# Kernel tuning notes

Hardware: AMD Instinct MI355X
Metric: run time of the kernel (lower is better)

The kernel has to match this reference:

```python
import jax, jax.numpy as jnp
import numpy as np

NEG_INF = -1e9


def setup_inputs() -> dict:
    key = jax.random.key(0)
    ks = jax.random.split(key, 12)
    B, Tq, Tki, E, D, M = 4, 2048, 2048, 1024, 128, 16384
    return {
        "x": jax.random.normal(ks[0], (B, Tq, E), jnp.float32),
        "ki": jax.random.normal(ks[1], (B, Tki, E), jnp.float32),
        "vi": jax.random.normal(ks[2], (B, Tki, E), jnp.float32),
        "mem_keys": jax.random.normal(ks[3], (B, M, D), jnp.float32),
        "mem_vals": jax.random.normal(ks[4], (B, M, D), jnp.float32),
        "Wq": jax.random.normal(ks[5], (E, D), jnp.float32) / np.sqrt(E),
        "bq": jax.random.normal(ks[6], (D,), jnp.float32) * 0.02,
        "Wk": jax.random.normal(ks[7], (E, D), jnp.float32) / np.sqrt(E),
        "bk": jax.random.normal(ks[8], (D,), jnp.float32) * 0.02,
        "Wv": jax.random.normal(ks[9], (E, D), jnp.float32) / np.sqrt(E),
        "bv": jax.random.normal(ks[10], (D,), jnp.float32) * 0.02,
        "gate": jax.random.normal(ks[11], (1,), jnp.float32),
        "idx": 3,
    }


def reference(x, ki, vi, mem_keys, mem_vals, Wq, bq, Wk, bk, Wv, bv, gate, idx):
    B, Tq, E = x.shape
    D = Wq.shape[1]
    top_k = 32
    q = x @ Wq + bq            # [B,Tq,D]
    k = x @ Wk + bk            # [B,Tq,D]
    v = x @ Wv + bv
    s = idx * D                # idx is a python int -> static slice
    k_full = jnp.concatenate([ki[:, :, s:s + D], k], axis=1)   # [B,Tk,D]
    v_full = jnp.concatenate([vi[:, :, s:s + D], v], axis=1)
    Tk = k_full.shape[1]
    # causal SDPA over prefix+current, offset diagonal Tk-Tq
    scores = jnp.einsum("bqd,bkd->bqk", q, k_full) / jnp.sqrt(jnp.float32(D))
    i = jnp.arange(Tq)[:, None]
    j = jnp.arange(Tk)[None, :]
    causal = j <= i + (Tk - Tq)
    scores = jnp.where(causal, scores, NEG_INF)
    att = jax.nn.softmax(scores, axis=-1)
    out = jnp.einsum("bqk,bkd->bqd", att, v_full)              # [B,Tq,D]
    # kNN memory attention: exact top-k inner-product search per query
    mem_scores = jnp.einsum("btd,bmd->btm", q, mem_keys)       # [B,Tq,M]
    _, top_idx = jax.lax.top_k(mem_scores, top_k)              # [B,Tq,K]
    gather = jax.vmap(lambda mem, ix: mem[ix])                 # per batch
    mem_k = gather(mem_keys, top_idx)                          # [B,Tq,K,D]
    mem_v = gather(mem_vals, top_idx)
    # note: original scales by sqrt(Cq)=sqrt(n_embd), not sqrt(head_size)
    mem_att = jax.nn.softmax(
        jnp.einsum("btd,btkd->btk", q, mem_k) / jnp.sqrt(jnp.float32(E)), axis=-1)
    mem_out = jnp.einsum("btk,btkd->btd", mem_att, mem_v)      # [B,Tq,D]
    md_out = out * gate + mem_out * (1.0 - gate)
    return md_out
```

## Files before the change

kernel.cpp:

```cpp
#include <hip/hip_runtime.h>


using bf16x8 = __attribute__((ext_vector_type(8))) short;
using f32x4  = __attribute__((ext_vector_type(4))) float;

typedef __attribute__((address_space(1))) const void GVoid;
typedef __attribute__((address_space(3))) void LVoid;
__device__ __forceinline__ void gl16(const ushort* g, ushort* l) {
  __builtin_amdgcn_global_load_lds((GVoid*)g, (LVoid*)l, 16, 0, 0);
}

__device__ __forceinline__ float bf2f(ushort h) {
  union { uint u; float f; } x; x.u = ((uint)h) << 16; return x.f;
}
__device__ __forceinline__ ushort f2bf(float f) {
  union { float f; uint u; } x; x.f = f;
  uint u = x.u;
  u += 0x7fffu + ((u >> 16) & 1u);
  return (ushort)(u >> 16);
}
__device__ __forceinline__ uint ord2(uint v) {
  uint s = (v >> 15) & 0x00010001u;
  uint t = (s << 15) - s;
  return v ^ t ^ 0x80008000u;
}
__device__ __forceinline__ ushort ord1(ushort h) {
  uint s = (h >> 15) & 1u;
  return (ushort)(h ^ ((s << 15) - s) ^ 0x8000u);
}

__global__ __launch_bounds__(256) void k_wt(const float* __restrict__ Wq,
                                            const float* __restrict__ Wk,
                                            const float* __restrict__ Wv,
                                            ushort* __restrict__ Wth,
                                            ushort* __restrict__ Wtlq) {
  int id = blockIdx.x * 256 + threadIdx.x;
  int z = id >> 17, r = id & 131071;
  int n = r >> 10, k = r & 1023;
  const float* W = (z == 1) ? Wk : (z == 2) ? Wv : Wq;
  float w = W[k * 128 + n];
  ushort h = f2bf(w);
  if (z < 3) Wth[id] = h;
  else       Wtlq[r] = f2bf(w - bf2f(h));
}

__global__ __launch_bounds__(256) void k_cvt8(const float* __restrict__ src,
                                              ushort* __restrict__ dst) {
  int id = blockIdx.x * 256 + threadIdx.x;
  size_t base = (size_t)id * 8;
  float4 a = *(const float4*)(src + base);
  float4 b = *(const float4*)(src + base + 4);
  bf16x8 r;
  r[0] = (short)f2bf(a.x); r[1] = (short)f2bf(a.y);
  r[2] = (short)f2bf(a.z); r[3] = (short)f2bf(a.w);
  r[4] = (short)f2bf(b.x); r[5] = (short)f2bf(b.y);
  r[6] = (short)f2bf(b.z); r[7] = (short)f2bf(b.w);
  *(bf16x8*)(dst + base) = r;
}

__global__ __launch_bounds__(256) void k_xsplit(const float* __restrict__ x,
                                                ushort* __restrict__ xh,
                                                ushort* __restrict__ xl) {
  int id = blockIdx.x * 256 + threadIdx.x;
  size_t base = (size_t)id * 8;
  float4 a = *(const float4*)(x + base);
  float4 b = *(const float4*)(x + base + 4);
  float xf[8] = {a.x, a.y, a.z, a.w, b.x, b.y, b.z, b.w};
  bf16x8 rh, rl;
#pragma unroll
  for (int j = 0; j < 8; ++j) {
    ushort h = f2bf(xf[j]);
    rh[j] = (short)h;
    rl[j] = (short)f2bf(xf[j] - bf2f(h));
  }
  *(bf16x8*)(xh + base) = rh;
  *(bf16x8*)(xl + base) = rl;
}

__global__ __launch_bounds__(256) void k_prefix(const float* __restrict__ ki,
                                                const float* __restrict__ vi,
                                                const int* __restrict__ idx,
                                                ushort* __restrict__ kfull,
                                                ushort* __restrict__ vfull) {
  int s = idx[0] * 128;
  int id = blockIdx.x * 256 + threadIdx.x;
  int d8 = (id & 15) * 8;
  int bt = id >> 4;
  int b = bt >> 11, t = bt & 2047;
  const float* kp = ki + (size_t)bt * 1024 + s + d8;
  const float* vp = vi + (size_t)bt * 1024 + s + d8;
  bf16x8 rk, rv;
#pragma unroll
  for (int j = 0; j < 8; ++j) { rk[j] = (short)f2bf(kp[j]); rv[j] = (short)f2bf(vp[j]); }
  size_t dst = ((size_t)b * 4096 + t) * 128 + d8;
  *(bf16x8*)(kfull + dst) = rk;
  *(bf16x8*)(vfull + dst) = rv;
}

__global__ __launch_bounds__(256) void k_qkv3(const ushort* __restrict__ xh,
                                              const ushort* __restrict__ xl,
                                              const ushort* __restrict__ Wth,
                                              const ushort* __restrict__ Wtlq,
                                              const float* __restrict__ bq,
                                              const float* __restrict__ bk,
                                              const float* __restrict__ bv,
                                              float* __restrict__ qex,
                                              ushort* __restrict__ kfull,
                                              ushort* __restrict__ vfull) {
  __shared__ ushort lds[2][16384];
  int z = blockIdx.z;
  int g = blockIdx.y;
  int m0 = blockIdx.x * 64;
  int tid = threadIdx.x;
  int w = tid >> 6, lane = tid & 63;
  int l15 = lane & 15, q8 = (lane >> 4) * 8;
  const ushort* Wz = Wth + (size_t)z * 131072;
  const ushort* xh_src = xh + (size_t)(m0 + w * 16 + l15) * 1024 + q8;
  const ushort* xl_src = xl + (size_t)(m0 + w * 16 + l15) * 1024 + q8;
  const ushort* wh_src = Wz   + (size_t)(g * 64 + w * 16 + l15) * 1024 + q8;
  const ushort* wl_src = Wtlq + (size_t)(g * 64 + w * 16 + l15) * 1024 + q8;
  int sb = w * 1024;

  f32x4 zero = {0.f, 0.f, 0.f, 0.f};
  f32x4 acc[4] = {zero, zero, zero, zero};

  {
    ushort* B = &lds[0][0];
    gl16(xh_src,      B + sb);
    gl16(xh_src + 32, B + sb + 512);
    gl16(wh_src,      B + 8192 + sb);
    gl16(wh_src + 32, B + 8192 + sb + 512);
    if (z == 0) {
      gl16(xl_src,      B + 4096 + sb);
      gl16(xl_src + 32, B + 4096 + sb + 512);
      gl16(wl_src,      B + 12288 + sb);
      gl16(wl_src + 32, B + 12288 + sb + 512);
    }
  }
  __syncthreads();
  int bf = 0;
  for (int t16 = 0; t16 < 16; ++t16) {
    if (t16 < 15) {
      int k0 = t16 * 64 + 64;
      ushort* B = &lds[bf ^ 1][0];
      gl16(xh_src + k0,      B + sb);
      gl16(xh_src + k0 + 32, B + sb + 512);
      gl16(wh_src + k0,      B + 8192 + sb);
      gl16(wh_src + k0 + 32, B + 8192 + sb + 512);
      if (z == 0) {
        gl16(xl_src + k0,      B + 4096 + sb);
        gl16(xl_src + k0 + 32, B + 4096 + sb + 512);
        gl16(wl_src + k0,      B + 12288 + sb);
        gl16(wl_src + k0 + 32, B + 12288 + sb + 512);
      }
    }
    const ushort* B = &lds[bf][0];
    int lo = lane * 8;
    if (z == 0) {
#pragma unroll
      for (int kc = 0; kc < 2; ++kc) {
        bf16x8 ah = *(const bf16x8*)(B + (w * 2 + kc) * 512 + lo);
        bf16x8 al = *(const bf16x8*)(B + 4096 + (w * 2 + kc) * 512 + lo);
#pragma unroll
        for (int cc = 0; cc < 4; ++cc) {
          bf16x8 bh = *(const bf16x8*)(B + 8192 + (cc * 2 + kc) * 512 + lo);
          bf16x8 bl = *(const bf16x8*)(B + 12288 + (cc * 2 + kc) * 512 + lo);
          acc[cc] = __builtin_amdgcn_mfma_f32_16x16x32_bf16(ah, bh, acc[cc], 0, 0, 0);
          acc[cc] = __builtin_amdgcn_mfma_f32_16x16x32_bf16(ah, bl, acc[cc], 0, 0, 0);
          acc[cc] = __builtin_amdgcn_mfma_f32_16x16x32_bf16(al, bh, acc[cc], 0, 0, 0);
        }
      }
    } else {
#pragma unroll
      for (int kc = 0; kc < 2; ++kc) {
        bf16x8 ah = *(const bf16x8*)(B + (w * 2 + kc) * 512 + lo);
#pragma unroll
        for (int cc = 0; cc < 4; ++cc) {
          bf16x8 bh = *(const bf16x8*)(B + 8192 + (cc * 2 + kc) * 512 + lo);
          acc[cc] = __builtin_amdgcn_mfma_f32_16x16x32_bf16(ah, bh, acc[cc], 0, 0, 0);
        }
      }
    }
    __syncthreads();
    bf ^= 1;
  }

  const float* bias = (z == 0) ? bq : (z == 1) ? bk : bv;
  int mrow = m0 + w * 16 + (lane >> 4) * 4;
#pragma unroll
  for (int cc = 0; cc < 4; ++cc) {
    int n = g * 64 + cc * 16 + l15;
    float bb = bias[n];
#pragma unroll
    for (int r = 0; r < 4; ++r) {
      int m = mrow + r;
      float val = acc[cc][r] + bb;
      if (z == 0) {
        qex[(size_t)m * 128 + n] = val;
      } else {
        int b2 = m >> 11, tt = m & 2047;
        size_t o = ((size_t)b2 * 4096 + 2048 + tt) * 128 + n;
        if (z == 1) kfull[o] = f2bf(val); else vfull[o] = f2bf(val);
      }
    }
  }
}

__global__ __launch_bounds__(256) void k_vt(const ushort* __restrict__ vfull,
                                            ushort* __restrict__ Vt) {
  __shared__ ushort lds[64][136];
  int blk = blockIdx.x;
  int b = blk >> 6, t0 = (blk & 63) * 64;
  int t = threadIdx.x;
#pragma unroll
  for (int p = 0; p < 4; ++p) {
    int ch = p * 256 + t;
    int row = ch >> 4, c8 = (ch & 15) * 8;
    uint4 v = *(const uint4*)(vfull + ((size_t)b * 4096 + t0 + row) * 128 + c8);
    *(uint4*)(&lds[row][c8]) = v;
  }
  __syncthreads();
#pragma unroll
  for (int p = 0; p < 8; ++p) {
    int q = p * 256 + t;
    int d = q >> 4, t4 = (q & 15) * 4;
    ushort4 o;
    o.x = lds[t4 + 0][d]; o.y = lds[t4 + 1][d];
    o.z = lds[t4 + 2][d]; o.w = lds[t4 + 3][d];
    *(ushort4*)(Vt + ((size_t)b * 128 + d) * 4096 + t0 + t4) = o;
  }
}

__global__ __launch_bounds__(256) void k_scores(const float* __restrict__ A,
                                                const ushort* __restrict__ Bm,
                                                ushort* __restrict__ S,
                                                ushort* __restrict__ cmax,
                                                int N, int nslice, int causalOff,
                                                long sA, long sB, long sS) {
  __shared__ ushort Bt[64 * 136];
  int q0 = blockIdx.x * 64;
  int ns0 = blockIdx.y * nslice;
  int nend = ns0 + nslice; if (nend > N) nend = N;
  int climit = q0 + 64 + causalOff; if (nend > climit) nend = climit;
  if (ns0 >= nend) return;
  int zb = blockIdx.z;
  const float*  Ab = A  + (size_t)zb * sA;
  const ushort* Bb = Bm + (size_t)zb * sB;
  ushort* Sb = S + (size_t)zb * sS;
  int t = threadIdx.x, lane = t & 63, wv = t >> 6;
  int l15 = lane & 15, q8 = (lane >> 4) * 8;
  const float* Arow = Ab + (size_t)(q0 + wv * 16 + l15) * 128 + q8;
  bf16x8 af[4];
#pragma unroll
  for (int kc = 0; kc < 4; ++kc)
#pragma unroll
    for (int j = 0; j < 8; ++j) af[kc][j] = (short)f2bf(Arow[kc * 32 + j]);
  for (int n0 = ns0; n0 < nend; n0 += 64) {
#pragma unroll
    for (int p = 0; p < 4; ++p) {
      int ch = p * 256 + t;
      int row = ch >> 4, c8 = (ch & 15) * 8;
      uint4 v = *(const uint4*)(Bb + (size_t)(n0 + row) * 128 + c8);
      *(uint4*)(&Bt[row * 136 + c8]) = v;
    }
    __syncthreads();
    f32x4 zero = {0.f, 0.f, 0.f, 0.f};
    f32x4 acc[4] = {zero, zero, zero, zero};
#pragma unroll
    for (int h = 0; h < 4; ++h) {
#pragma unroll
      for (int kc = 0; kc < 4; ++kc) {
        bf16x8 bfr = *(const bf16x8*)(&Bt[(h * 16 + l15) * 136 + kc * 32 + q8]);
        acc[h] = __builtin_amdgcn_mfma_f32_16x16x32_bf16(af[kc], bfr, acc[h], 0, 0, 0);
      }
    }
    int qq = q0 + wv * 16 + (lane >> 4) * 4;
#pragma unroll
    for (int h = 0; h < 4; ++h)
#pragma unroll
      for (int r = 0; r < 4; ++r)
        Sb[(size_t)(qq + r) * N + (n0 + h * 16 + l15)] = f2bf(acc[h][r]);
    if (cmax) {
#pragma unroll
      for (int r = 0; r < 4; ++r) {
        float m = fmaxf(fmaxf(acc[0][r], acc[1][r]), fmaxf(acc[2][r], acc[3][r]));
#pragma unroll
        for (int off = 1; off < 16; off <<= 1) m = fmaxf(m, __shfl_xor(m, off));
        if (l15 == 0)
          cmax[(size_t)(qq + r) * 256 + (n0 >> 6)] = ord1(f2bf(m));
      }
    }
    __syncthreads();
  }
}

__global__ __launch_bounds__(256) void k_softmax(ushort* __restrict__ S) {
  int rid = blockIdx.x;
  int i = rid & 2047;
  ushort* row = S + (size_t)rid * 4096;
  int w = i + 2049;
  int t = threadIdx.x;
  const float scale = 0.08838834764831845f;
  float v[16];
  float mx = -1e30f;
#pragma unroll
  for (int c = 0; c < 16; ++c) {
    int e = c * 256 + t;
    float f = -1e30f;
    if (e < w) f = bf2f(row[e]) * scale;
    v[c] = f;
    mx = fmaxf(mx, f);
  }
  __shared__ float red[4];
#pragma unroll
  for (int off = 32; off; off >>= 1) mx = fmaxf(mx, __shfl_xor(mx, off));
  if ((t & 63) == 0) red[t >> 6] = mx;
  __syncthreads();
  mx = fmaxf(fmaxf(red[0], red[1]), fmaxf(red[2], red[3]));
  __syncthreads();
  float ex[16];
  float sum = 0.f;
#pragma unroll
  for (int c = 0; c < 16; ++c) {
    int e = c * 256 + t;
    ex[c] = (e < w) ? __expf(v[c] - mx) : 0.f;
    sum += ex[c];
  }
#pragma unroll
  for (int off = 32; off; off >>= 1) sum += __shfl_xor(sum, off);
  if ((t & 63) == 0) red[t >> 6] = sum;
  __syncthreads();
  sum = red[0] + red[1] + red[2] + red[3];
  float inv = 1.f / sum;
#pragma unroll
  for (int c = 0; c < 16; ++c) {
    int e = c * 256 + t;
    row[e] = f2bf(ex[c] * inv);
  }
}

__global__ __launch_bounds__(128) void k_pv(const ushort* __restrict__ P,
                                            const ushort* __restrict__ Vt,
                                            float* __restrict__ O) {
  __shared__ ushort lds[2][4096];
  int b = blockIdx.z;
  int d0 = blockIdx.y * 32;
  int q0 = blockIdx.x * 32;
  int t = threadIdx.x, lane = t & 63, w = t >> 6;
  int l15 = lane & 15, q8 = (lane >> 4) * 8;
  const ushort* Pq = P + ((size_t)b * 2048 + q0) * 4096;
  const ushort* Vb = Vt + (size_t)b * 128 * 4096;
  const ushort* p_src = Pq + (size_t)(w * 16 + l15) * 4096 + q8;
  const ushort* v_src = Vb + (size_t)(d0 + w * 16 + l15) * 4096 + q8;
  int kend = q0 + 32 + 2048; if (kend > 4096) kend = 4096;
  int ksteps = (kend + 63) >> 6;

  f32x4 zero = {0.f, 0.f, 0.f, 0.f};
  f32x4 acc[2] = {zero, zero};

  {
    ushort* B = &lds[0][0];
    gl16(p_src,      B + (w * 2 + 0) * 512);
    gl16(p_src + 32, B + (w * 2 + 1) * 512);
    gl16(v_src,      B + 2048 + (w * 2 + 0) * 512);
    gl16(v_src + 32, B + 2048 + (w * 2 + 1) * 512);
  }
  __syncthreads();
  int bf = 0;
  for (int st = 0; st < ksteps; ++st) {
    if (st + 1 < ksteps) {
      int k0 = st * 64 + 64;
      ushort* B = &lds[bf ^ 1][0];
      gl16(p_src + k0,      B + (w * 2 + 0) * 512);
      gl16(p_src + k0 + 32, B + (w * 2 + 1) * 512);
      gl16(v_src + k0,      B + 2048 + (w * 2 + 0) * 512);
      gl16(v_src + k0 + 32, B + 2048 + (w * 2 + 1) * 512);
    }
    const ushort* B = &lds[bf][0];
    int lo = lane * 8;
#pragma unroll
    for (int kc = 0; kc < 2; ++kc) {
      bf16x8 af = *(const bf16x8*)(B + (w * 2 + kc) * 512 + lo);
#pragma unroll
      for (int nc = 0; nc < 2; ++nc) {
        bf16x8 bfr = *(const bf16x8*)(B + 2048 + (nc * 2 + kc) * 512 + lo);
        acc[nc] = __builtin_amdgcn_mfma_f32_16x16x32_bf16(af, bfr, acc[nc], 0, 0, 0);
      }
    }
    __syncthreads();
    bf ^= 1;
  }

  size_t ob = ((size_t)b * 2048 + q0 + w * 16 + (lane >> 4) * 4) * 128;
#pragma unroll
  for (int nc = 0; nc < 2; ++nc)
#pragma unroll
    for (int r = 0; r < 4; ++r)
      O[ob + (size_t)r * 128 + d0 + nc * 16 + l15] = acc[nc][r];
}

__global__ __launch_bounds__(256) void k_topk(const ushort* __restrict__ Sall,
                                              const ushort* __restrict__ cmaxA,
                                              const float* __restrict__ qf32b,
                                              const float* __restrict__ memk,
                                              const float* __restrict__ memv,
                                              float* __restrict__ mout) {
  __shared__ ushort marr[256];
  __shared__ ushort chun[256];
  __shared__ float qf[128];
  __shared__ uint cidx[384];
  __shared__ float csc[384];
  __shared__ unsigned long long ckey[384];
  __shared__ uint selIdx[32];
  __shared__ float selS[32];
  __shared__ float obuf[256];
  __shared__ int nF, nC;
  __shared__ uint sT;

  int i = blockIdx.x;
  const ushort* Srow = Sall + (size_t)i * 16384;
  int t = threadIdx.x;
  int wv = t >> 6, lane = t & 63;
  if (t < 128) qf[t] = qf32b[(size_t)i * 128 + t];
  if (t == 0) { nF = 0; nC = 0; }
  uint cm = cmaxA[(size_t)i * 256 + t];
  marr[t] = (ushort)cm;
  __syncthreads();

  {
    int rank = 0;
#pragma unroll 8
    for (int j = 0; j < 256; ++j) {
      uint vj = marr[j];
      rank += (vj > cm) || (vj == cm && j < t);
    }
    if (rank == 63) sT = cm;
  }
  __syncthreads();
  uint T = sT;
  if (cm >= T) { int p = atomicAdd(&nF, 1); chun[p] = (ushort)t; }
  __syncthreads();
  int F = nF;

  for (int jj = (t >> 3); jj < F; jj += 32) {
    int base = ((int)chun[jj]) * 64 + (t & 7) * 8;
    uint4 rv = *(const uint4*)(Srow + base);
    uint a0 = ord2(rv.x), a1 = ord2(rv.y), a2 = ord2(rv.z), a3 = ord2(rv.w);
    if ((a0 & 0xffffu) >= T) { int p = atomicAdd(&nC, 1); if (p < 384) cidx[p] = (uint)(base + 0); }
    if ((a0 >> 16)     >= T) { int p = atomicAdd(&nC, 1); if (p < 384) cidx[p] = (uint)(base + 1); }
    if ((a1 & 0xffffu) >= T) { int p = atomicAdd(&nC, 1); if (p < 384) cidx[p] = (uint)(base + 2); }
    if ((a1 >> 16)     >= T) { int p = atomicAdd(&nC, 1); if (p < 384) cidx[p] = (uint)(base + 3); }
    if ((a2 & 0xffffu) >= T) { int p = atomicAdd(&nC, 1); if (p < 384) cidx[p] = (uint)(base + 4); }
    if ((a2 >> 16)     >= T) { int p = atomicAdd(&nC, 1); if (p < 384) cidx[p] = (uint)(base + 5); }
    if ((a3 & 0xffffu) >= T) { int p = atomicAdd(&nC, 1); if (p < 384) cidx[p] = (uint)(base + 6); }
    if ((a3 >> 16)     >= T) { int p = atomicAdd(&nC, 1); if (p < 384) cidx[p] = (uint)(base + 7); }
  }
  __syncthreads();
  int C = nC; if (C > 384) C = 384;

  {
    float qa = qf[lane * 2], qb = qf[lane * 2 + 1];
    for (int j0 = wv; j0 < C; j0 += 32) {
      float2 pp[8];
      float s[8];
#pragma unroll
      for (int u = 0; u < 8; ++u) {
        int j = j0 + u * 4;
        if (j < C) pp[u] = *(const float2*)(memk + (size_t)cidx[j] * 128 + lane * 2);
      }
#pragma unroll
      for (int u = 0; u < 8; ++u) {
        int j = j0 + u * 4;
        s[u] = (j < C) ? (qa * pp[u].x + qb * pp[u].y) : 0.f;
      }
#pragma unroll
      for (int off = 32; off; off >>= 1) {
#pragma unroll
        for (int u = 0; u < 8; ++u) s[u] += __shfl_xor(s[u], off);
      }
      if (lane == 0) {
#pragma unroll
        for (int u = 0; u < 8; ++u) {
          int j = j0 + u * 4;
          if (j < C) csc[j] = s[u];
        }
      }
    }
  }
  __syncthreads();
  for (int j = t; j < C; j += 256) {
    uint sb2 = __float_as_uint(csc[j]);
    uint o = (sb2 & 0x80000000u) ? ~sb2 : (sb2 | 0x80000000u);
    ckey[j] = ((unsigned long long)o << 32) | (uint)(~cidx[j]);
  }
  __syncthreads();
  for (int j = t; j < C; j += 256) {
    unsigned long long my = ckey[j];
    int rank = 0;
    for (int l = 0; l < C; ++l) rank += (ckey[l] > my) ? 1 : 0;
    if (rank < 32) { selS[rank] = csc[j]; selIdx[rank] = cidx[j]; }
  }
  __syncthreads();
  if (wv == 0) {
    float sc = (lane < 32) ? selS[lane] * 0.03125f : -1e30f;
    float mx = sc;
#pragma unroll
    for (int off = 32; off; off >>= 1) mx = fmaxf(mx, __shfl_xor(mx, off));
    float ex = (lane < 32) ? __expf(sc - mx) : 0.f;
    float Z = ex;
#pragma unroll
    for (int off = 32; off; off >>= 1) Z += __shfl_xor(Z, off);
    if (lane < 32) selS[lane] = ex / Z;
  }
  __syncthreads();
  {
    int d = t & 127, half = t >> 7;
    float vv[16];
#pragma unroll
    for (int u = 0; u < 16; ++u)
      vv[u] = memv[(size_t)selIdx[half * 16 + u] * 128 + d];
    float acc = 0.f;
#pragma unroll
    for (int u = 0; u < 16; ++u)
      acc += selS[half * 16 + u] * vv[u];
    obuf[t] = acc;
  }
  __syncthreads();
  if (t < 128) mout[(size_t)i * 128 + t] = obuf[t] + obuf[t + 128];
}

__global__ __launch_bounds__(256) void k_mix(const float* __restrict__ a,
                                             const float* __restrict__ b,
                                             const float* __restrict__ gate,
                                             float* __restrict__ out) {
  int id = blockIdx.x * 256 + threadIdx.x;
  float g = gate[0];
  float4 va = ((const float4*)a)[id];
  float4 vb = ((const float4*)b)[id];
  float4 o;
  o.x = va.x * g + vb.x * (1.f - g);
  o.y = va.y * g + vb.y * (1.f - g);
  o.z = va.z * g + vb.z * (1.f - g);
  o.w = va.w * g + vb.w * (1.f - g);
  ((float4*)out)[id] = o;
}

extern "C" void kernel_launch(void* const* d_in, const int* in_sizes, int n_in,
                              void* d_out, int out_size, void* d_ws, size_t ws_size,
                              hipStream_t stream) {
  const float* x    = (const float*)d_in[0];
  const float* ki   = (const float*)d_in[1];
  const float* vi   = (const float*)d_in[2];
  const float* mk   = (const float*)d_in[3];
  const float* mv   = (const float*)d_in[4];
  const float* Wq   = (const float*)d_in[5];
  const float* bq   = (const float*)d_in[6];
  const float* Wk   = (const float*)d_in[7];
  const float* bk   = (const float*)d_in[8];
  const float* Wv   = (const float*)d_in[9];
  const float* bv   = (const float*)d_in[10];
  const float* gate = (const float*)d_in[11];
  const int*   idx  = (const int*)d_in[12];

  char* ws = (char*)d_ws;
  ushort* Sbuf  = (ushort*)(ws);
  ushort* xh    = (ushort*)(ws);
  ushort* xl    = (ushort*)(ws + 16777216);
  float*  qex   = (float*) (ws + 67108864);
  ushort* kfull = (ushort*)(ws + 71303168);
  ushort* vfull = (ushort*)(ws + 75497472);
  ushort* Vt    = (ushort*)(ws + 79691776);
  ushort* mkb   = (ushort*)(ws + 83886080);
  ushort* Wth   = (ushort*)(ws + 100663296);
  ushort* Wtlq  = (ushort*)(ws + 101449728);
  float*  osdpa = (float*) (ws + 101711872);
  float*  mout  = (float*) (ws + 105906176);
  ushort* cmaxb = (ushort*)(ws + 110100480);

  k_wt<<<2048, 256, 0, stream>>>(Wq, Wk, Wv, Wth, Wtlq);
  k_cvt8<<<4096, 256, 0, stream>>>(mk, mkb);
  k_xsplit<<<4096, 256, 0, stream>>>(x, xh, xl);
  k_prefix<<<512, 256, 0, stream>>>(ki, vi, idx, kfull, vfull);

  k_qkv3<<<dim3(128, 2, 3), 256, 0, stream>>>(xh, xl, Wth, Wtlq, bq, bk, bv,
                                              qex, kfull, vfull);
  k_vt<<<256, 256, 0, stream>>>(vfull, Vt);

  k_scores<<<dim3(32, 8, 4), 256, 0, stream>>>(qex, kfull, Sbuf, nullptr,
                                               4096, 512, 2048,
                                               (long)2048 * 128, (long)4096 * 128,
                                               (long)2048 * 4096);
  k_softmax<<<8192, 256, 0, stream>>>(Sbuf);
  k_pv<<<dim3(64, 4, 4), 128, 0, stream>>>(Sbuf, Vt, osdpa);

  for (int b = 0; b < 4; ++b) {
    k_scores<<<dim3(32, 32, 1), 256, 0, stream>>>(qex + (size_t)b * 2048 * 128,
                                                  mkb + (size_t)b * 16384 * 128,
                                                  Sbuf, cmaxb,
                                                  16384, 512, (1 << 28),
                                                  0, 0, 0);
    k_topk<<<2048, 256, 0, stream>>>(Sbuf, cmaxb,
                                     qex + (size_t)b * 2048 * 128,
                                     mk + (size_t)b * 16384 * 128,
                                     mv + (size_t)b * 16384 * 128,
                                     mout + (size_t)b * 2048 * 128);
  }

  k_mix<<<1024, 256, 0, stream>>>(osdpa, mout, gate, (float*)d_out);
}
```

Baseline: 611.2 us.

## Double-buffer score-kernel B tiles with async global-to-LDS loads and XOR swizzle

Changes k_scores to stage the key tile into LDS with global_load_lds direct copies into two buffers, prefetching the next 64-row tile while MFMAs run on the current one. The padded layout is replaced by an XOR-swizzled 128-wide layout so reads avoid bank conflicts without padding. This is meant to hide global load latency and remove the register round trip and one barrier per iteration. It doubles LDS use per block, which may lower occupancy, and relies on the async loads being complete at the trailing barrier.

```diff
diff --git a/kernel.cpp b/kernel.cpp
--- a/kernel.cpp
+++ b/kernel.cpp
@@ -237,7 +237,7 @@
                                                 ushort* __restrict__ cmax,
                                                 int N, int nslice, int causalOff,
                                                 long sA, long sB, long sS) {
-  __shared__ ushort Bt[64 * 136];
+  __shared__ __align__(16) ushort Bt[2][8192];
   int q0 = blockIdx.x * 64;
   int ns0 = blockIdx.y * nslice;
   int nend = ns0 + nslice; if (nend > N) nend = N;
@@ -255,22 +255,40 @@
   for (int kc = 0; kc < 4; ++kc)
 #pragma unroll
     for (int j = 0; j < 8; ++j) af[kc][j] = (short)f2bf(Arow[kc * 32 + j]);
+  int srow[4], soff[4];
+#pragma unroll
+  for (int i = 0; i < 4; ++i) {
+    int br = wv * 16 + i * 4;
+    int rr = br + (lane >> 4);
+    int c  = (l15) ^ (rr & 7);
+    srow[i] = rr;
+    soff[i] = c * 8;
+  }
+  {
+#pragma unroll
+    for (int i = 0; i < 4; ++i)
+      gl16(Bb + (size_t)(ns0 + srow[i]) * 128 + soff[i],
+           &Bt[0][(wv * 16 + i * 4) * 128]);
+  }
+  __syncthreads();
+  int bf = 0;
   for (int n0 = ns0; n0 < nend; n0 += 64) {
-#pragma unroll
-    for (int p = 0; p < 4; ++p) {
-      int ch = p * 256 + t;
-      int row = ch >> 4, c8 = (ch & 15) * 8;
-      uint4 v = *(const uint4*)(Bb + (size_t)(n0 + row) * 128 + c8);
-      *(uint4*)(&Bt[row * 136 + c8]) = v;
-    }
-    __syncthreads();
+    if (n0 + 64 < nend) {
+#pragma unroll
+      for (int i = 0; i < 4; ++i)
+        gl16(Bb + (size_t)(n0 + 64 + srow[i]) * 128 + soff[i],
+             &Bt[bf ^ 1][(wv * 16 + i * 4) * 128]);
+    }
+    const ushort* B = &Bt[bf][0];
     f32x4 zero = {0.f, 0.f, 0.f, 0.f};
     f32x4 acc[4] = {zero, zero, zero, zero};
 #pragma unroll
     for (int h = 0; h < 4; ++h) {
 #pragma unroll
       for (int kc = 0; kc < 4; ++kc) {
-        bf16x8 bfr = *(const bf16x8*)(&Bt[(h * 16 + l15) * 136 + kc * 32 + q8]);
+        int row = h * 16 + l15;
+        int p = (kc * 4 + (lane >> 4)) ^ (row & 7);
+        bf16x8 bfr = *(const bf16x8*)(B + row * 128 + p * 8);
         acc[h] = __builtin_amdgcn_mfma_f32_16x16x32_bf16(af[kc], bfr, acc[h], 0, 0, 0);
       }
     }
@@ -291,6 +309,7 @@
       }
     }
     __syncthreads();
+    bf ^= 1;
   }
 }
 
```

After: 605.4 us. No clear change (-1.0%).
